# Kernel optimization log

Measured on AMD Instinct MI355X. Metric: run time of the kernel, lower is better.

## Reference

```python
import jax, jax.numpy as jnp
import numpy as np

B, T, F = 8192, 30, 16
H1, H2 = 64, 32


def _lstm(x, Wih, Whh, b):
    """PyTorch-convention LSTM (gate order i,f,g,o). x: [B,T,I] -> (ys [B,T,H], hT [B,H])."""
    H = Whh.shape[1]
    h0 = jnp.zeros((x.shape[0], H), x.dtype)

    def step(carry, xt):
        h, c = carry
        z = xt @ Wih.T + h @ Whh.T + b  # [B,4H]
        i, f, g, o = jnp.split(z, 4, axis=-1)
        c = jax.nn.sigmoid(f) * c + jax.nn.sigmoid(i) * jnp.tanh(g)
        h = jax.nn.sigmoid(o) * jnp.tanh(c)
        return (h, c), h

    (hT, _), ys = jax.lax.scan(step, (h0, h0), jnp.swapaxes(x, 0, 1))
    return jnp.swapaxes(ys, 0, 1), hT


def setup_inputs() -> dict:
    key = jax.random.key(0)
    ks = jax.random.split(key, 16)
    s = 0.1  # small init scale for numerical sanity
    return {
        "x": jax.random.normal(ks[0], (B, T, F), jnp.float32),
        "Wih1": jax.random.normal(ks[1], (4 * H1, F), jnp.float32) * s,
        "Whh1": jax.random.normal(ks[2], (4 * H1, H1), jnp.float32) * s,
        "b1": jax.random.normal(ks[3], (4 * H1,), jnp.float32) * s,
        "Wih2": jax.random.normal(ks[4], (4 * H2, H1), jnp.float32) * s,
        "Whh2": jax.random.normal(ks[5], (4 * H2, H2), jnp.float32) * s,
        "b2": jax.random.normal(ks[6], (4 * H2,), jnp.float32) * s,
        "Wih3": jax.random.normal(ks[7], (4 * H2, H2), jnp.float32) * s,
        "Whh3": jax.random.normal(ks[8], (4 * H2, H2), jnp.float32) * s,
        "b3": jax.random.normal(ks[9], (4 * H2,), jnp.float32) * s,
        "Wih4": jax.random.normal(ks[10], (4 * H1, H2), jnp.float32) * s,
        "Whh4": jax.random.normal(ks[11], (4 * H1, H1), jnp.float32) * s,
        "b4": jax.random.normal(ks[12], (4 * H1,), jnp.float32) * s,
        "Wout": jax.random.normal(ks[13], (F, H1), jnp.float32) * s,
        "bout": jax.random.normal(ks[14], (F,), jnp.float32) * s,
    }


def reference(x, Wih1, Whh1, b1, Wih2, Whh2, b2, Wih3, Whh3, b3, Wih4, Whh4, b4, Wout, bout):
    ys1, _ = _lstm(x, Wih1, Whh1, b1)          # encoder LSTM(64)
    _, latent = _lstm(ys1, Wih2, Whh2, b2)      # encoder LSTM(32) -> final hidden [B,32]
    repeated = jnp.broadcast_to(latent[:, None, :], (latent.shape[0], T, latent.shape[1]))
    ys3, _ = _lstm(repeated, Wih3, Whh3, b3)    # decoder LSTM(32)
    ys4, _ = _lstm(ys3, Wih4, Whh4, b4)         # decoder LSTM(64)
    return ys4 @ Wout.T + bout                  # [B,T,F]
```

## Files before the change

kernel.cpp:

```cpp
#include <hip/hip_runtime.h>


#define TT 30
#define FF 16

typedef unsigned short u16t;
typedef __attribute__((ext_vector_type(8))) short short8;
typedef __attribute__((ext_vector_type(4))) short short4v;
typedef __attribute__((ext_vector_type(4))) float floatx4;

#define MFMA(a, b, c) __builtin_amdgcn_mfma_f32_16x16x32_bf16(a, b, c, 0, 0, 0)

template <int P> struct IC { static constexpr int v = P; };

__device__ __forceinline__ float rcpf(float v) { return __builtin_amdgcn_rcpf(v); }
__device__ __forceinline__ float sigf(float v) { return rcpf(1.f + __expf(-v)); }
__device__ __forceinline__ float tanhf_(float v) { return 1.f - 2.f * rcpf(1.f + __expf(2.f * v)); }
__device__ __forceinline__ u16t f2bf(float f) {
  unsigned int u = __float_as_uint(f);
  u = (u + 0x7FFFu + ((u >> 16) & 1u)) >> 16;
  return (u16t)u;
}
__device__ __forceinline__ short8 ldFrag(const float* p) {
  const float4 lo = *(const float4*)p;
  const float4 hi = *(const float4*)(p + 4);
  short8 r;
  r[0] = (short)f2bf(lo.x); r[1] = (short)f2bf(lo.y);
  r[2] = (short)f2bf(lo.z); r[3] = (short)f2bf(lo.w);
  r[4] = (short)f2bf(hi.x); r[5] = (short)f2bf(hi.y);
  r[6] = (short)f2bf(hi.z); r[7] = (short)f2bf(hi.w);
  return r;
}
__device__ __forceinline__ float cellUp(const floatx4 acc, float& c) {
  float iv = sigf(acc[0]), fv = sigf(acc[1]);
  float gv = tanhf_(acc[2]), ov = sigf(acc[3]);
  c = fv * c + iv * gv;
  return ov * tanhf_(c);
}

__global__ __launch_bounds__(512, 4) void lstm_ae_mfma5(
    const float* __restrict__ x,
    const float* __restrict__ Wih1, const float* __restrict__ Whh1, const float* __restrict__ b1,
    const float* __restrict__ Wih2, const float* __restrict__ Whh2, const float* __restrict__ b2,
    const float* __restrict__ Wih3, const float* __restrict__ Whh3, const float* __restrict__ b3,
    const float* __restrict__ Wih4, const float* __restrict__ Whh4, const float* __restrict__ b4,
    const float* __restrict__ Wout, const float* __restrict__ bout,
    float* __restrict__ out)
{
  __shared__ __align__(16) u16t xAll[16 * 968];
  __shared__ __align__(16) u16t aB[16 * 264];

  const int t = threadIdx.x;
  const int w = t >> 6, lane = t & 63;
  const int q = lane >> 4, n = lane & 15;
  const int q8 = q * 8, n264 = n * 264, n968 = n * 968;
  const int bBase = blockIdx.x * 16;
  const int nlo = n >> 2, ngt = n & 3;
  const u16t* aRow = &aB[n264];

  for (int i = t; i < 16 * 264; i += 512) aB[i] = 0;
  {
    const float* xb = x + (size_t)bBase * (TT * FF);
    for (int i4 = t; i4 < 1920; i4 += 512) {
      int e = i4 * 4;
      int b = e / 480, r = e - b * 480;
      int stp = r >> 4, f = r & 15;
      float4 v = *(const float4*)&xb[e];
      short4v s4 = { (short)f2bf(v.x), (short)f2bf(v.y), (short)f2bf(v.z), (short)f2bf(v.w) };
      *(short4v*)&xAll[b * 968 + stp * 32 + f] = s4;
    }
    for (int i = t; i < 7680; i += 512) {
      int b = i / 480, r = i - b * 480;
      int stp = r >> 4, f = r & 15;
      xAll[b * 968 + stp * 32 + 16 + f] = 0;
    }
  }
  short8 w1f[2][3]; floatx4 bias1[2];
  const short8 z8 = { 0, 0, 0, 0, 0, 0, 0, 0 };
#pragma unroll
  for (int tt = 0; tt < 2; ++tt) {
    int row = ngt * 64 + (2 * w + tt) * 4 + nlo;
    w1f[tt][0] = z8;
    if (q < 2) w1f[tt][0] = ldFrag(&Wih1[row * 16 + q8]);
    w1f[tt][1] = ldFrag(&Whh1[row * 64 + q8]);
    w1f[tt][2] = ldFrag(&Whh1[row * 64 + 32 + q8]);
#pragma unroll
    for (int r = 0; r < 4; ++r) bias1[tt][r] = b1[r * 64 + (2 * w + tt) * 4 + q];
  }
  short8 w2f[3]; floatx4 bias2;
  {
    int row = ngt * 32 + w * 4 + nlo;
    w2f[0] = ldFrag(&Wih2[row * 64 + q8]);
    w2f[1] = ldFrag(&Wih2[row * 64 + 32 + q8]);
    w2f[2] = ldFrag(&Whh2[row * 32 + q8]);
#pragma unroll
    for (int r = 0; r < 4; ++r) bias2[r] = b2[r * 32 + w * 4 + q];
  }
  if (blockIdx.x & 256) {
    __builtin_amdgcn_s_sleep(15);
    __builtin_amdgcn_s_sleep(15);
  }
  __syncthreads();

  float c1v[2] = {0.f, 0.f}, c2v = 0.f;

  {
    const short8 bx = *(const short8*)&xAll[n968 + q8];
    floatx4 a0 = bias1[0], a1 = bias1[1];
    a0 = MFMA(w1f[0][0], bx, a0); a1 = MFMA(w1f[1][0], bx, a1);
    aB[n264 + (2 * w) * 4 + q]     = f2bf(cellUp(a0, c1v[0]));
    aB[n264 + (2 * w + 1) * 4 + q] = f2bf(cellUp(a1, c1v[1]));
  }
  short8 bxN = *(const short8*)&xAll[n968 + 32 + q8];
  __syncthreads();

  auto stepA = [&](int st, auto pc) {
    constexpr int p = decltype(pc)::v;
    const short8 bh1a = *(const short8*)&aRow[p * 64 + q8];
    const short8 bh1b = *(const short8*)&aRow[p * 64 + 32 + q8];
    const short8 bh2  = *(const short8*)&aRow[128 + (1 - p) * 32 + q8];
    floatx4 a2 = bias2;
    a2 = MFMA(w2f[0], bh1a, a2);
    a2 = MFMA(w2f[1], bh1b, a2);
    a2 = MFMA(w2f[2], bh2, a2);
    floatx4 a0 = bias1[0], a1 = bias1[1];
    a0 = MFMA(w1f[0][0], bxN, a0);  a1 = MFMA(w1f[1][0], bxN, a1);
    a0 = MFMA(w1f[0][1], bh1a, a0); a1 = MFMA(w1f[1][1], bh1a, a1);
    a0 = MFMA(w1f[0][2], bh1b, a0); a1 = MFMA(w1f[1][2], bh1b, a1);
    const int nx = (st + 2 < TT) ? st + 2 : TT - 1;
    bxN = *(const short8*)&xAll[n968 + nx * 32 + q8];
    aB[n264 + 128 + p * 32 + w * 4 + q]           = f2bf(cellUp(a2, c2v));
    aB[n264 + (1 - p) * 64 + (2 * w) * 4 + q]     = f2bf(cellUp(a0, c1v[0]));
    aB[n264 + (1 - p) * 64 + (2 * w + 1) * 4 + q] = f2bf(cellUp(a1, c1v[1]));
    __syncthreads();
  };
  for (int st = 0; st < 28; st += 2) { stepA(st, IC<0>{}); stepA(st + 1, IC<1>{}); }
  stepA(28, IC<0>{});
  {
    const short8 bh1a = *(const short8*)&aRow[64 + q8];
    const short8 bh1b = *(const short8*)&aRow[96 + q8];
    const short8 bh2  = *(const short8*)&aRow[128 + q8];
    floatx4 a2 = bias2;
    a2 = MFMA(w2f[0], bh1a, a2);
    a2 = MFMA(w2f[1], bh1b, a2);
    a2 = MFMA(w2f[2], bh2, a2);
    aB[n264 + 160 + w * 4 + q] = f2bf(cellUp(a2, c2v));
  }
  __syncthreads();

  short8 w3f[2]; floatx4 bias3;
  {
    int row = ngt * 32 + w * 4 + nlo;
    w3f[0] = ldFrag(&Wih3[row * 32 + q8]);
    w3f[1] = ldFrag(&Whh3[row * 32 + q8]);
#pragma unroll
    for (int r = 0; r < 4; ++r) bias3[r] = b3[r * 32 + w * 4 + q];
  }
  short8 w4f[2][3]; floatx4 bias4[2];
#pragma unroll
  for (int tt = 0; tt < 2; ++tt) {
    int row = ngt * 64 + (2 * w + tt) * 4 + nlo;
    w4f[tt][0] = ldFrag(&Wih4[row * 32 + q8]);
    w4f[tt][1] = ldFrag(&Whh4[row * 64 + q8]);
    w4f[tt][2] = ldFrag(&Whh4[row * 64 + 32 + q8]);
#pragma unroll
    for (int r = 0; r < 4; ++r) bias4[tt][r] = b4[r * 64 + (2 * w + tt) * 4 + q];
  }
  short8 wof[2];
  wof[0] = ldFrag(&Wout[n * 64 + q8]);
  wof[1] = ldFrag(&Wout[n * 64 + 32 + q8]);
  const floatx4 biasO = *(const floatx4*)&bout[q * 4];
  const short8 blat = *(const short8*)&aRow[160 + q8];
  for (int i = t; i < 1024; i += 512) aB[(i >> 6) * 264 + 64 + (i & 63)] = 0;
  __syncthreads();

  float c3v = 0.f, c4v[2] = {0.f, 0.f};

  {
    floatx4 a3 = bias3;
    a3 = MFMA(w3f[0], blat, a3);
    aB[n264 + 192 + w * 4 + q] = f2bf(cellUp(a3, c3v));
  }
  __syncthreads();

  auto stepB = [&](int st, auto pc) {
    constexpr int p = decltype(pc)::v;
    const short8 bh3  = *(const short8*)&aRow[192 + p * 32 + q8];
    const short8 bh4a = *(const short8*)&aRow[(1 - p) * 64 + q8];
    const short8 bh4b = *(const short8*)&aRow[(1 - p) * 64 + 32 + q8];
    floatx4 a40 = bias4[0], a41 = bias4[1];
    a40 = MFMA(w4f[0][0], bh3, a40);  a41 = MFMA(w4f[1][0], bh3, a41);
    a40 = MFMA(w4f[0][1], bh4a, a40); a41 = MFMA(w4f[1][1], bh4a, a41);
    a40 = MFMA(w4f[0][2], bh4b, a40); a41 = MFMA(w4f[1][2], bh4b, a41);
    floatx4 a3 = bias3;
    a3 = MFMA(w3f[0], blat, a3);
    a3 = MFMA(w3f[1], bh3, a3);
    aB[n264 + p * 64 + (2 * w) * 4 + q]     = f2bf(cellUp(a40, c4v[0]));
    aB[n264 + p * 64 + (2 * w + 1) * 4 + q] = f2bf(cellUp(a41, c4v[1]));
    aB[n264 + 192 + (1 - p) * 32 + w * 4 + q] = f2bf(cellUp(a3, c3v));
    if (st > 0 && w == ((st - 1) & 7)) {
      floatx4 yv = biasO;
      yv = MFMA(wof[0], bh4a, yv);
      yv = MFMA(wof[1], bh4b, yv);
      *(floatx4*)&out[((size_t)(bBase + n) * TT + (st - 1)) * FF + q * 4] = yv;
    }
    __syncthreads();
  };
  for (int st = 0; st < 28; st += 2) { stepB(st, IC<0>{}); stepB(st + 1, IC<1>{}); }
  stepB(28, IC<0>{});
  {
    const short8 bh3  = *(const short8*)&aRow[224 + q8];
    const short8 bh4a = *(const short8*)&aRow[q8];
    const short8 bh4b = *(const short8*)&aRow[32 + q8];
    floatx4 a40 = bias4[0], a41 = bias4[1];
    a40 = MFMA(w4f[0][0], bh3, a40);  a41 = MFMA(w4f[1][0], bh3, a41);
    a40 = MFMA(w4f[0][1], bh4a, a40); a41 = MFMA(w4f[1][1], bh4a, a41);
    a40 = MFMA(w4f[0][2], bh4b, a40); a41 = MFMA(w4f[1][2], bh4b, a41);
    aB[n264 + 64 + (2 * w) * 4 + q]     = f2bf(cellUp(a40, c4v[0]));
    aB[n264 + 64 + (2 * w + 1) * 4 + q] = f2bf(cellUp(a41, c4v[1]));
    if (w == 4) {
      floatx4 yv = biasO;
      yv = MFMA(wof[0], bh4a, yv);
      yv = MFMA(wof[1], bh4b, yv);
      *(floatx4*)&out[((size_t)(bBase + n) * TT + 28) * FF + q * 4] = yv;
    }
  }
  __syncthreads();
  if (w == 5) {
    const short8 ba = *(const short8*)&aRow[64 + q8];
    const short8 bb = *(const short8*)&aRow[96 + q8];
    floatx4 yv = biasO;
    yv = MFMA(wof[0], ba, yv);
    yv = MFMA(wof[1], bb, yv);
    *(floatx4*)&out[((size_t)(bBase + n) * TT + 29) * FF + q * 4] = yv;
  }
}

extern "C" void kernel_launch(void* const* d_in, const int* in_sizes, int n_in,
                              void* d_out, int out_size, void* d_ws, size_t ws_size,
                              hipStream_t stream) {
  const float* x    = (const float*)d_in[0];
  const float* Wih1 = (const float*)d_in[1];
  const float* Whh1 = (const float*)d_in[2];
  const float* b1   = (const float*)d_in[3];
  const float* Wih2 = (const float*)d_in[4];
  const float* Whh2 = (const float*)d_in[5];
  const float* b2   = (const float*)d_in[6];
  const float* Wih3 = (const float*)d_in[7];
  const float* Whh3 = (const float*)d_in[8];
  const float* b3   = (const float*)d_in[9];
  const float* Wih4 = (const float*)d_in[10];
  const float* Whh4 = (const float*)d_in[11];
  const float* b4   = (const float*)d_in[12];
  const float* Wout = (const float*)d_in[13];
  const float* bout = (const float*)d_in[14];
  float* out = (float*)d_out;

  const int B = in_sizes[0] / (TT * FF);
  dim3 grid(B / 16), block(512);
  lstm_ae_mfma5<<<grid, block, 0, stream>>>(
      x, Wih1, Whh1, b1, Wih2, Whh2, b2, Wih3, Whh3, b3,
      Wih4, Whh4, b4, Wout, bout, out);
}
```

Baseline: 169.3 us.

## Split paired LSTM layers across dedicated warps and fold exp2 scaling into weights

Raises the block to 768 threads (12 waves). Waves 0-7 handle the 64-wide layers (1 and 4) and waves 8-11 handle the 32-wide layers (2 and 3), so the paired layers run on separate waves instead of being interleaved serially in every wave. Weights and biases are pre-scaled by log2(e), or 2·log2(e) for the g gate, so the activations can call the native exp2 directly without a multiply. This trades a shorter per-step critical path for more threads per block and divergent roles, which may lower occupancy and leaves the same barrier count per step.

```diff
diff --git a/kernel.cpp b/kernel.cpp
--- a/kernel.cpp
+++ b/kernel.cpp
@@ -3,6 +3,7 @@
 
 #define TT 30
 #define FF 16
+#define NT 768
 
 typedef unsigned short u16t;
 typedef __attribute__((ext_vector_type(8))) short short8;
@@ -11,34 +12,41 @@
 
 #define MFMA(a, b, c) __builtin_amdgcn_mfma_f32_16x16x32_bf16(a, b, c, 0, 0, 0)
 
+#if __has_builtin(__builtin_amdgcn_exp2f)
+#define EXP2(x) __builtin_amdgcn_exp2f(x)
+#else
+#define EXP2(x) exp2f(x)
+#endif
+
 template <int P> struct IC { static constexpr int v = P; };
 
 __device__ __forceinline__ float rcpf(float v) { return __builtin_amdgcn_rcpf(v); }
-__device__ __forceinline__ float sigf(float v) { return rcpf(1.f + __expf(-v)); }
-__device__ __forceinline__ float tanhf_(float v) { return 1.f - 2.f * rcpf(1.f + __expf(2.f * v)); }
 __device__ __forceinline__ u16t f2bf(float f) {
   unsigned int u = __float_as_uint(f);
   u = (u + 0x7FFFu + ((u >> 16) & 1u)) >> 16;
   return (u16t)u;
 }
-__device__ __forceinline__ short8 ldFrag(const float* p) {
+__device__ __forceinline__ short8 ldFragS(const float* p, float s) {
   const float4 lo = *(const float4*)p;
   const float4 hi = *(const float4*)(p + 4);
   short8 r;
-  r[0] = (short)f2bf(lo.x); r[1] = (short)f2bf(lo.y);
-  r[2] = (short)f2bf(lo.z); r[3] = (short)f2bf(lo.w);
-  r[4] = (short)f2bf(hi.x); r[5] = (short)f2bf(hi.y);
-  r[6] = (short)f2bf(hi.z); r[7] = (short)f2bf(hi.w);
+  r[0] = (short)f2bf(lo.x * s); r[1] = (short)f2bf(lo.y * s);
+  r[2] = (short)f2bf(lo.z * s); r[3] = (short)f2bf(lo.w * s);
+  r[4] = (short)f2bf(hi.x * s); r[5] = (short)f2bf(hi.y * s);
+  r[6] = (short)f2bf(hi.z * s); r[7] = (short)f2bf(hi.w * s);
   return r;
 }
 __device__ __forceinline__ float cellUp(const floatx4 acc, float& c) {
-  float iv = sigf(acc[0]), fv = sigf(acc[1]);
-  float gv = tanhf_(acc[2]), ov = sigf(acc[3]);
+  float iv = rcpf(1.f + EXP2(-acc[0]));
+  float fv = rcpf(1.f + EXP2(-acc[1]));
+  float gv = 1.f - 2.f * rcpf(1.f + EXP2(acc[2]));
+  float ov = rcpf(1.f + EXP2(-acc[3]));
   c = fv * c + iv * gv;
-  return ov * tanhf_(c);
-}
-
-__global__ __launch_bounds__(512, 4) void lstm_ae_mfma5(
+  float th = 1.f - 2.f * rcpf(1.f + EXP2(2.885390082f * c));
+  return ov * th;
+}
+
+__global__ __launch_bounds__(NT, 6) void lstm_ae_mfma6(
     const float* __restrict__ x,
     const float* __restrict__ Wih1, const float* __restrict__ Whh1, const float* __restrict__ b1,
     const float* __restrict__ Wih2, const float* __restrict__ Whh2, const float* __restrict__ b2,
@@ -57,11 +65,16 @@
   const int bBase = blockIdx.x * 16;
   const int nlo = n >> 2, ngt = n & 3;
   const u16t* aRow = &aB[n264];
-
-  for (int i = t; i < 16 * 264; i += 512) aB[i] = 0;
+  const bool isZ1 = (w < 8);
+  const int u = w & 3;
+
+  const float L1 = 1.442695041f, L2 = 2.885390082f;
+  const float sA = (ngt == 2) ? L2 : L1;
+
+  for (int i = t; i < 16 * 264; i += NT) aB[i] = 0;
   {
     const float* xb = x + (size_t)bBase * (TT * FF);
-    for (int i4 = t; i4 < 1920; i4 += 512) {
+    for (int i4 = t; i4 < 1920; i4 += NT) {
       int e = i4 * 4;
       int b = e / 480, r = e - b * 480;
       int stp = r >> 4, f = r & 15;
@@ -69,32 +82,37 @@
       short4v s4 = { (short)f2bf(v.x), (short)f2bf(v.y), (short)f2bf(v.z), (short)f2bf(v.w) };
       *(short4v*)&xAll[b * 968 + stp * 32 + f] = s4;
     }
-    for (int i = t; i < 7680; i += 512) {
+    for (int i = t; i < 7680; i += NT) {
       int b = i / 480, r = i - b * 480;
       int stp = r >> 4, f = r & 15;
       xAll[b * 968 + stp * 32 + 16 + f] = 0;
     }
   }
-  short8 w1f[2][3]; floatx4 bias1[2];
   const short8 z8 = { 0, 0, 0, 0, 0, 0, 0, 0 };
-#pragma unroll
-  for (int tt = 0; tt < 2; ++tt) {
-    int row = ngt * 64 + (2 * w + tt) * 4 + nlo;
-    w1f[tt][0] = z8;
-    if (q < 2) w1f[tt][0] = ldFrag(&Wih1[row * 16 + q8]);
-    w1f[tt][1] = ldFrag(&Whh1[row * 64 + q8]);
-    w1f[tt][2] = ldFrag(&Whh1[row * 64 + 32 + q8]);
-#pragma unroll
-    for (int r = 0; r < 4; ++r) bias1[tt][r] = b1[r * 64 + (2 * w + tt) * 4 + q];
-  }
-  short8 w2f[3]; floatx4 bias2;
-  {
-    int row = ngt * 32 + w * 4 + nlo;
-    w2f[0] = ldFrag(&Wih2[row * 64 + q8]);
-    w2f[1] = ldFrag(&Wih2[row * 64 + 32 + q8]);
-    w2f[2] = ldFrag(&Whh2[row * 32 + q8]);
-#pragma unroll
-    for (int r = 0; r < 4; ++r) bias2[r] = b2[r * 32 + w * 4 + q];
+  short8 wAf[2][3]; floatx4 biasA[2];
+  if (isZ1) {
+#pragma unroll
+    for (int tt = 0; tt < 2; ++tt) {
+      int T = w + 8 * tt;
+      int row = ngt * 64 + T * 4 + nlo;
+      wAf[tt][0] = z8;
+      if (q < 2) wAf[tt][0] = ldFragS(&Wih1[row * 16 + q8], sA);
+      wAf[tt][1] = ldFragS(&Whh1[row * 64 + q8], sA);
+      wAf[tt][2] = ldFragS(&Whh1[row * 64 + 32 + q8], sA);
+#pragma unroll
+      for (int r = 0; r < 4; ++r) biasA[tt][r] = b1[r * 64 + T * 4 + q] * (r == 2 ? L2 : L1);
+    }
+  } else {
+#pragma unroll
+    for (int tt = 0; tt < 2; ++tt) {
+      int T = 2 * u + tt;
+      int row = ngt * 32 + T * 4 + nlo;
+      wAf[tt][0] = ldFragS(&Wih2[row * 64 + q8], sA);
+      wAf[tt][1] = ldFragS(&Wih2[row * 64 + 32 + q8], sA);
+      wAf[tt][2] = ldFragS(&Whh2[row * 32 + q8], sA);
+#pragma unroll
+      for (int r = 0; r < 4; ++r) biasA[tt][r] = b2[r * 32 + T * 4 + q] * (r == 2 ? L2 : L1);
+    }
   }
   if (blockIdx.x & 256) {
     __builtin_amdgcn_s_sleep(15);
@@ -102,122 +120,155 @@
   }
   __syncthreads();
 
-  float c1v[2] = {0.f, 0.f}, c2v = 0.f;
-
-  {
+  float cA[2] = {0.f, 0.f};
+  short8 bxN;
+
+  if (isZ1) {
     const short8 bx = *(const short8*)&xAll[n968 + q8];
-    floatx4 a0 = bias1[0], a1 = bias1[1];
-    a0 = MFMA(w1f[0][0], bx, a0); a1 = MFMA(w1f[1][0], bx, a1);
-    aB[n264 + (2 * w) * 4 + q]     = f2bf(cellUp(a0, c1v[0]));
-    aB[n264 + (2 * w + 1) * 4 + q] = f2bf(cellUp(a1, c1v[1]));
-  }
-  short8 bxN = *(const short8*)&xAll[n968 + 32 + q8];
+#pragma unroll
+    for (int tt = 0; tt < 2; ++tt) {
+      floatx4 a0 = biasA[tt];
+      a0 = MFMA(wAf[tt][0], bx, a0);
+      aB[n264 + (w + 8 * tt) * 4 + q] = f2bf(cellUp(a0, cA[tt]));
+    }
+    bxN = *(const short8*)&xAll[n968 + 32 + q8];
+  }
   __syncthreads();
 
   auto stepA = [&](int st, auto pc) {
     constexpr int p = decltype(pc)::v;
     const short8 bh1a = *(const short8*)&aRow[p * 64 + q8];
     const short8 bh1b = *(const short8*)&aRow[p * 64 + 32 + q8];
-    const short8 bh2  = *(const short8*)&aRow[128 + (1 - p) * 32 + q8];
-    floatx4 a2 = bias2;
-    a2 = MFMA(w2f[0], bh1a, a2);
-    a2 = MFMA(w2f[1], bh1b, a2);
-    a2 = MFMA(w2f[2], bh2, a2);
-    floatx4 a0 = bias1[0], a1 = bias1[1];
-    a0 = MFMA(w1f[0][0], bxN, a0);  a1 = MFMA(w1f[1][0], bxN, a1);
-    a0 = MFMA(w1f[0][1], bh1a, a0); a1 = MFMA(w1f[1][1], bh1a, a1);
-    a0 = MFMA(w1f[0][2], bh1b, a0); a1 = MFMA(w1f[1][2], bh1b, a1);
-    const int nx = (st + 2 < TT) ? st + 2 : TT - 1;
-    bxN = *(const short8*)&xAll[n968 + nx * 32 + q8];
-    aB[n264 + 128 + p * 32 + w * 4 + q]           = f2bf(cellUp(a2, c2v));
-    aB[n264 + (1 - p) * 64 + (2 * w) * 4 + q]     = f2bf(cellUp(a0, c1v[0]));
-    aB[n264 + (1 - p) * 64 + (2 * w + 1) * 4 + q] = f2bf(cellUp(a1, c1v[1]));
+    if (isZ1) {
+#pragma unroll
+      for (int tt = 0; tt < 2; ++tt) {
+        floatx4 a0 = biasA[tt];
+        a0 = MFMA(wAf[tt][0], bxN, a0);
+        a0 = MFMA(wAf[tt][1], bh1a, a0);
+        a0 = MFMA(wAf[tt][2], bh1b, a0);
+        aB[n264 + (1 - p) * 64 + (w + 8 * tt) * 4 + q] = f2bf(cellUp(a0, cA[tt]));
+      }
+      const int nx = (st + 2 < TT) ? st + 2 : TT - 1;
+      bxN = *(const short8*)&xAll[n968 + nx * 32 + q8];
+    } else {
+      const short8 bh2 = *(const short8*)&aRow[128 + (1 - p) * 32 + q8];
+#pragma unroll
+      for (int tt = 0; tt < 2; ++tt) {
+        floatx4 a2 = biasA[tt];
+        a2 = MFMA(wAf[tt][0], bh1a, a2);
+        a2 = MFMA(wAf[tt][1], bh1b, a2);
+        a2 = MFMA(wAf[tt][2], bh2, a2);
+        aB[n264 + 128 + p * 32 + (2 * u + tt) * 4 + q] = f2bf(cellUp(a2, cA[tt]));
+      }
+    }
     __syncthreads();
   };
   for (int st = 0; st < 28; st += 2) { stepA(st, IC<0>{}); stepA(st + 1, IC<1>{}); }
   stepA(28, IC<0>{});
-  {
+  if (!isZ1) {
     const short8 bh1a = *(const short8*)&aRow[64 + q8];
     const short8 bh1b = *(const short8*)&aRow[96 + q8];
     const short8 bh2  = *(const short8*)&aRow[128 + q8];
-    floatx4 a2 = bias2;
-    a2 = MFMA(w2f[0], bh1a, a2);
-    a2 = MFMA(w2f[1], bh1b, a2);
-    a2 = MFMA(w2f[2], bh2, a2);
-    aB[n264 + 160 + w * 4 + q] = f2bf(cellUp(a2, c2v));
-  }
-  __syncthreads();
-
-  short8 w3f[2]; floatx4 bias3;
-  {
-    int row = ngt * 32 + w * 4 + nlo;
-    w3f[0] = ldFrag(&Wih3[row * 32 + q8]);
-    w3f[1] = ldFrag(&Whh3[row * 32 + q8]);
-#pragma unroll
-    for (int r = 0; r < 4; ++r) bias3[r] = b3[r * 32 + w * 4 + q];
-  }
-  short8 w4f[2][3]; floatx4 bias4[2];
-#pragma unroll
-  for (int tt = 0; tt < 2; ++tt) {
-    int row = ngt * 64 + (2 * w + tt) * 4 + nlo;
-    w4f[tt][0] = ldFrag(&Wih4[row * 32 + q8]);
-    w4f[tt][1] = ldFrag(&Whh4[row * 64 + q8]);
-    w4f[tt][2] = ldFrag(&Whh4[row * 64 + 32 + q8]);
-#pragma unroll
-    for (int r = 0; r < 4; ++r) bias4[tt][r] = b4[r * 64 + (2 * w + tt) * 4 + q];
-  }
-  short8 wof[2];
-  wof[0] = ldFrag(&Wout[n * 64 + q8]);
-  wof[1] = ldFrag(&Wout[n * 64 + 32 + q8]);
-  const floatx4 biasO = *(const floatx4*)&bout[q * 4];
-  const short8 blat = *(const short8*)&aRow[160 + q8];
-  for (int i = t; i < 1024; i += 512) aB[(i >> 6) * 264 + 64 + (i & 63)] = 0;
-  __syncthreads();
-
-  float c3v = 0.f, c4v[2] = {0.f, 0.f};
-
-  {
-    floatx4 a3 = bias3;
-    a3 = MFMA(w3f[0], blat, a3);
-    aB[n264 + 192 + w * 4 + q] = f2bf(cellUp(a3, c3v));
+#pragma unroll
+    for (int tt = 0; tt < 2; ++tt) {
+      floatx4 a2 = biasA[tt];
+      a2 = MFMA(wAf[tt][0], bh1a, a2);
+      a2 = MFMA(wAf[tt][1], bh1b, a2);
+      a2 = MFMA(wAf[tt][2], bh2, a2);
+      aB[n264 + 160 + (2 * u + tt) * 4 + q] = f2bf(cellUp(a2, cA[tt]));
+    }
+  }
+  __syncthreads();
+
+  short8 wBf[2][3]; floatx4 biasB[2];
+  short8 wof[2]; floatx4 biasO;
+  short8 blat;
+  if (isZ1) {
+#pragma unroll
+    for (int tt = 0; tt < 2; ++tt) {
+      int T = w + 8 * tt;
+      int row = ngt * 64 + T * 4 + nlo;
+      wBf[tt][0] = ldFragS(&Wih4[row * 32 + q8], sA);
+      wBf[tt][1] = ldFragS(&Whh4[row * 64 + q8], sA);
+      wBf[tt][2] = ldFragS(&Whh4[row * 64 + 32 + q8], sA);
+#pragma unroll
+      for (int r = 0; r < 4; ++r) biasB[tt][r] = b4[r * 64 + T * 4 + q] * (r == 2 ? L2 : L1);
+    }
+    wof[0] = ldFragS(&Wout[n * 64 + q8], 1.f);
+    wof[1] = ldFragS(&Wout[n * 64 + 32 + q8], 1.f);
+    biasO = *(const floatx4*)&bout[q * 4];
+  } else {
+#pragma unroll
+    for (int tt = 0; tt < 2; ++tt) {
+      int T = 2 * u + tt;
+      int row = ngt * 32 + T * 4 + nlo;
+      wBf[tt][0] = ldFragS(&Wih3[row * 32 + q8], sA);
+      wBf[tt][1] = ldFragS(&Whh3[row * 32 + q8], sA);
+#pragma unroll
+      for (int r = 0; r < 4; ++r) biasB[tt][r] = b3[r * 32 + T * 4 + q] * (r == 2 ? L2 : L1);
+    }
+    blat = *(const short8*)&aRow[160 + q8];
+  }
+  for (int i = t; i < 1024; i += NT) aB[(i >> 6) * 264 + 64 + (i & 63)] = 0;
+  __syncthreads();
+
+  float cB[2] = {0.f, 0.f};
+
+  if (!isZ1) {
+#pragma unroll
+    for (int tt = 0; tt < 2; ++tt) {
+      floatx4 a3 = biasB[tt];
+      a3 = MFMA(wBf[tt][0], blat, a3);
+      aB[n264 + 192 + (2 * u + tt) * 4 + q] = f2bf(cellUp(a3, cB[tt]));
+    }
   }
   __syncthreads();
 
   auto stepB = [&](int st, auto pc) {
     constexpr int p = decltype(pc)::v;
-    const short8 bh3  = *(const short8*)&aRow[192 + p * 32 + q8];
-    const short8 bh4a = *(const short8*)&aRow[(1 - p) * 64 + q8];
-    const short8 bh4b = *(const short8*)&aRow[(1 - p) * 64 + 32 + q8];
-    floatx4 a40 = bias4[0], a41 = bias4[1];
-    a40 = MFMA(w4f[0][0], bh3, a40);  a41 = MFMA(w4f[1][0], bh3, a41);
-    a40 = MFMA(w4f[0][1], bh4a, a40); a41 = MFMA(w4f[1][1], bh4a, a41);
-    a40 = MFMA(w4f[0][2], bh4b, a40); a41 = MFMA(w4f[1][2], bh4b, a41);
-    floatx4 a3 = bias3;
-    a3 = MFMA(w3f[0], blat, a3);
-    a3 = MFMA(w3f[1], bh3, a3);
-    aB[n264 + p * 64 + (2 * w) * 4 + q]     = f2bf(cellUp(a40, c4v[0]));
-    aB[n264 + p * 64 + (2 * w + 1) * 4 + q] = f2bf(cellUp(a41, c4v[1]));
-    aB[n264 + 192 + (1 - p) * 32 + w * 4 + q] = f2bf(cellUp(a3, c3v));
-    if (st > 0 && w == ((st - 1) & 7)) {
-      floatx4 yv = biasO;
-      yv = MFMA(wof[0], bh4a, yv);
-      yv = MFMA(wof[1], bh4b, yv);
-      *(floatx4*)&out[((size_t)(bBase + n) * TT + (st - 1)) * FF + q * 4] = yv;
+    const short8 bh3 = *(const short8*)&aRow[192 + p * 32 + q8];
+    if (isZ1) {
+      const short8 bh4a = *(const short8*)&aRow[(1 - p) * 64 + q8];
+      const short8 bh4b = *(const short8*)&aRow[(1 - p) * 64 + 32 + q8];
+#pragma unroll
+      for (int tt = 0; tt < 2; ++tt) {
+        floatx4 a4 = biasB[tt];
+        a4 = MFMA(wBf[tt][0], bh3, a4);
+        a4 = MFMA(wBf[tt][1], bh4a, a4);
+        a4 = MFMA(wBf[tt][2], bh4b, a4);
+        aB[n264 + p * 64 + (w + 8 * tt) * 4 + q] = f2bf(cellUp(a4, cB[tt]));
+      }
+      if (st > 0 && w == ((st - 1) & 7)) {
+        floatx4 yv = biasO;
+        yv = MFMA(wof[0], bh4a, yv);
+        yv = MFMA(wof[1], bh4b, yv);
+        *(floatx4*)&out[((size_t)(bBase + n) * TT + (st - 1)) * FF + q * 4] = yv;
+      }
+    } else {
+#pragma unroll
+      for (int tt = 0; tt < 2; ++tt) {
+        floatx4 a3 = biasB[tt];
+        a3 = MFMA(wBf[tt][0], blat, a3);
+        a3 = MFMA(wBf[tt][1], bh3, a3);
+        aB[n264 + 192 + (1 - p) * 32 + (2 * u + tt) * 4 + q] = f2bf(cellUp(a3, cB[tt]));
+      }
     }
     __syncthreads();
   };
   for (int st = 0; st < 28; st += 2) { stepB(st, IC<0>{}); stepB(st + 1, IC<1>{}); }
   stepB(28, IC<0>{});
-  {
+  if (isZ1) {
     const short8 bh3  = *(const short8*)&aRow[224 + q8];
     const short8 bh4a = *(const short8*)&aRow[q8];
     const short8 bh4b = *(const short8*)&aRow[32 + q8];
-    floatx4 a40 = bias4[0], a41 = bias4[1];
-    a40 = MFMA(w4f[0][0], bh3, a40);  a41 = MFMA(w4f[1][0], bh3, a41);
-    a40 = MFMA(w4f[0][1], bh4a, a40); a41 = MFMA(w4f[1][1], bh4a, a41);
-    a40 = MFMA(w4f[0][2], bh4b, a40); a41 = MFMA(w4f[1][2], bh4b, a41);
-    aB[n264 + 64 + (2 * w) * 4 + q]     = f2bf(cellUp(a40, c4v[0]));
-    aB[n264 + 64 + (2 * w + 1) * 4 + q] = f2bf(cellUp(a41, c4v[1]));
+#pragma unroll
+    for (int tt = 0; tt < 2; ++tt) {
+      floatx4 a4 = biasB[tt];
+      a4 = MFMA(wBf[tt][0], bh3, a4);
+      a4 = MFMA(wBf[tt][1], bh4a, a4);
+      a4 = MFMA(wBf[tt][2], bh4b, a4);
+      aB[n264 + 64 + (w + 8 * tt) * 4 + q] = f2bf(cellUp(a4, cB[tt]));
+    }
     if (w == 4) {
       floatx4 yv = biasO;
       yv = MFMA(wof[0], bh4a, yv);
@@ -257,8 +308,8 @@
   float* out = (float*)d_out;
 
   const int B = in_sizes[0] / (TT * FF);
-  dim3 grid(B / 16), block(512);
-  lstm_ae_mfma5<<<grid, block, 0, stream>>>(
+  dim3 grid(B / 16), block(NT);
+  lstm_ae_mfma6<<<grid, block, 0, stream>>>(
       x, Wih1, Whh1, b1, Wih2, Whh2, b2, Wih3, Whh3, b3,
       Wih4, Whh4, b4, Wout, bout, out);
 }
```

Result: no change. 169.4 us (+0.1%).
